# Optimization experiments

Measured on AMD Instinct MI355X. Metric: run time of the kernel, lower is better.

## Reference

```python
import jax, jax.numpy as jnp
import numpy as np

N = 20000      # nodes
E = 320000     # edges
GD = 256       # g_dim
H = 8          # head_n
D = 32         # head_d
XD = 256       # x_dim
PS = 4         # x_ps
HID = 512      # FF hidden (hardcoded in module)
EPS = 1e-5
SCALE = GD ** -0.5  # note: module scales by g_dim**-0.5, not head_d**-0.5


def layernorm(x, w, b):
    mu = jnp.mean(x, axis=-1, keepdims=True)
    var = jnp.var(x, axis=-1, keepdims=True)
    return (x - mu) * jax.lax.rsqrt(var + EPS) * w + b


def setup_inputs() -> dict:
    key = jax.random.key(0)
    ks = jax.random.split(key, 16)
    inp = {
        "x": jax.random.normal(ks[0], (N, XD, PS, PS), jnp.float32),
        "h": jax.random.normal(ks[1], (N, GD), jnp.float32),
        "src": jax.random.randint(ks[2], (E,), 0, N, jnp.int32),
        "dst": jax.random.randint(ks[3], (E,), 0, N, jnp.int32),
        # xproj conv (kernel covers full patch -> equivalent to a linear)
        "conv_w": jax.random.normal(ks[4], (GD, XD, PS, PS), jnp.float32) * 0.02,
        "conv_b": jnp.zeros((GD,), jnp.float32),
        # GraphT outer LayerNorm
        "norm_w": jnp.ones((GD,), jnp.float32),
        "norm_b": jnp.zeros((GD,), jnp.float32),
        # attention norm_in + projections
        "nin_w": jnp.ones((GD,), jnp.float32),
        "nin_b": jnp.zeros((GD,), jnp.float32),
        "w_qkv": jax.random.normal(ks[5], (3 * H * D, GD), jnp.float32) * 0.02,
        "w_out": jax.random.normal(ks[6], (GD, H * D), jnp.float32) * 0.02,
        "b_out": jnp.zeros((GD,), jnp.float32),
        # FeedForward: LayerNorm + Linear(GD,HID) + GELU + Linear(HID,GD)
        "ffn_w": jnp.ones((GD,), jnp.float32),
        "ffn_b": jnp.zeros((GD,), jnp.float32),
        "w1": jax.random.normal(ks[7], (HID, GD), jnp.float32) * 0.02,
        "b1": jnp.zeros((HID,), jnp.float32),
        "w2": jax.random.normal(ks[8], (GD, HID), jnp.float32) * 0.02,
        "b2": jnp.zeros((GD,), jnp.float32),
    }
    return inp


def reference(x, h, src, dst, conv_w, conv_b, norm_w, norm_b, nin_w, nin_b,
              w_qkv, w_out, b_out, ffn_w, ffn_b, w1, b1, w2, b2):
    # xproj: Conv2d with kernel == full spatial extent -> linear over flattened patch
    xp = x.reshape(N, XD * PS * PS) @ conv_w.reshape(GD, XD * PS * PS).T + conv_b  # [N, GD]

    hn = layernorm(h, norm_w, norm_b)  # GraphT.norm

    # --- GraphAttention ---
    s = layernorm(hn, nin_w, nin_b)                    # norm_in
    qkv = s @ w_qkv.T                                  # [N, 3*H*D]
    q, k, v = jnp.split(qkv, 3, axis=-1)
    q = q.reshape(N, H, D)
    k = k.reshape(N, H, D)
    v = v.reshape(N, H, D)

    # per-edge elementwise attention (DGL u_mul_v), scaled
    att = q[src] * k[dst] * SCALE                      # [E, H, D]
    # edge softmax over incoming edges of each destination, per (h, d) slot
    amax = jax.ops.segment_max(att, dst, num_segments=N)   # [N, H, D]
    e = jnp.exp(att - amax[dst])
    z = jax.ops.segment_sum(e, dst, num_segments=N)
    a = e / z[dst]                                     # [E, H, D]
    # weighted aggregation: sum over edges of v_src * att
    rst = jax.ops.segment_sum(v[src] * a, dst, num_segments=N)  # [N, H, D]

    attn_out = rst.reshape(N, H * D) @ w_out.T + b_out  # to_out (dropout=eval noop)

    # --- FeedForward (norm -> linear -> gelu -> linear) ---
    f = layernorm(attn_out, ffn_w, ffn_b)
    f = jax.nn.gelu(f @ w1.T + b1, approximate=False)
    f = f @ w2.T + b2

    out = f + hn + xp
    return out
```

## Files before the change

kernel.cpp:

```cpp
#include <hip/hip_runtime.h>
#include <hip/hip_bf16.h>
#include <math.h>

typedef __hip_bfloat16 bf16;
typedef __attribute__((ext_vector_type(8))) short bf16x8;
typedef __attribute__((ext_vector_type(4))) float f32x4;

#define N_NODES 20000
#define N_EDGES 320000
#define GD 256
#define HID 512
#define QKV3 768
#define SCALE 0.0625f
#define EPS 1e-5f

__device__ __forceinline__ float b2f(bf16 x) { return __bfloat162float(x); }
__device__ __forceinline__ bf16 f2b(float x) { return __float2bfloat16(x); }
__device__ __forceinline__ short f2bs(float x) {
    bf16 b = __float2bfloat16(x);
    union { bf16 b; short s; } u; u.b = b; return u.s;
}
__device__ __forceinline__ float ldf(const void* p, size_t i, int isbf) {
    return isbf ? __bfloat162float(((const bf16*)p)[i]) : ((const float*)p)[i];
}

__global__ void detect_kernel(const void* __restrict__ normw, int* __restrict__ flag) {
    if (threadIdx.x == 0) {
        unsigned short u = ((const unsigned short*)normw)[0];
        *flag = (u == 0x3F80) ? 1 : 0;
    }
}

struct ConvArgs {
    const void* src[5];
    bf16* dst[5];
    int n[5];
};
__global__ void conv_bf16_all(ConvArgs a, const int* __restrict__ flag) {
    int i = blockIdx.x * 256 + threadIdx.x;
    int fl = *flag;
    #pragma unroll
    for (int s = 0; s < 5; ++s) {
        if (i < a.n[s]) {
            a.dst[s][i] = f2b(ldf(a.src[s], i, fl));
            return;
        }
        i -= a.n[s];
    }
}

__global__ void count_kernel(const int* __restrict__ dst, int* __restrict__ deg) {
    int e = blockIdx.x * 256 + threadIdx.x;
    if (e < N_EDGES) atomicAdd(&deg[dst[e]], 1);
}

__global__ void scan_kernel(const int* __restrict__ deg, int* __restrict__ offsets,
                            int* __restrict__ cursor) {
    const int T = 1024;
    int t = threadIdx.x;
    int chunk = (N_NODES + T - 1) / T;
    int beg = t * chunk;
    int end = beg + chunk; if (end > N_NODES) end = N_NODES;
    int s = 0;
    for (int i = beg; i < end; ++i) s += deg[i];
    __shared__ int ls[T];
    ls[t] = s;
    __syncthreads();
    for (int off = 1; off < T; off <<= 1) {
        int v = (t >= off) ? ls[t - off] : 0;
        __syncthreads();
        ls[t] += v;
        __syncthreads();
    }
    int run = (t == 0) ? 0 : ls[t - 1];
    for (int i = beg; i < end; ++i) {
        offsets[i] = run; cursor[i] = run; run += deg[i];
    }
    if (t == T - 1) offsets[N_NODES] = run;
}

__global__ void fill_kernel(const int* __restrict__ src, const int* __restrict__ dst,
                            int* __restrict__ cursor, int* __restrict__ ssrc) {
    int e = blockIdx.x * 256 + threadIdx.x;
    if (e < N_EDGES) {
        int p = atomicAdd(&cursor[dst[e]], 1);
        ssrc[p] = src[e];
    }
}

__global__ void ln_fused_kernel(const void* __restrict__ h,
                                const void* __restrict__ nw, const void* __restrict__ nb,
                                const void* __restrict__ iw, const void* __restrict__ ib,
                                float* __restrict__ hn, bf16* __restrict__ s,
                                const int* __restrict__ flag) {
    int wave = threadIdx.x >> 6, lane = threadIdx.x & 63;
    int n = blockIdx.x * 4 + wave;
    int fl = *flag;
    size_t base = (size_t)n * GD;
    float x[4]; float sum = 0.f, sq = 0.f;
    #pragma unroll
    for (int i = 0; i < 4; ++i) {
        x[i] = ldf(h, base + lane + 64 * i, fl);
        sum += x[i]; sq += x[i] * x[i];
    }
    #pragma unroll
    for (int off = 32; off; off >>= 1) { sum += __shfl_xor(sum, off); sq += __shfl_xor(sq, off); }
    float mu = sum * (1.0f / GD);
    float rs = rsqrtf(sq * (1.0f / GD) - mu * mu + EPS);
    float y[4]; float s2 = 0.f, q2 = 0.f;
    #pragma unroll
    for (int i = 0; i < 4; ++i) {
        int j = lane + 64 * i;
        y[i] = (x[i] - mu) * rs * ldf(nw, j, fl) + ldf(nb, j, fl);
        hn[base + j] = y[i];
        s2 += y[i]; q2 += y[i] * y[i];
    }
    #pragma unroll
    for (int off = 32; off; off >>= 1) { s2 += __shfl_xor(s2, off); q2 += __shfl_xor(q2, off); }
    float mu2 = s2 * (1.0f / GD);
    float rs2 = rsqrtf(q2 * (1.0f / GD) - mu2 * mu2 + EPS);
    #pragma unroll
    for (int i = 0; i < 4; ++i) {
        int j = lane + 64 * i;
        s[base + j] = f2b((y[i] - mu2) * rs2 * ldf(iw, j, fl) + ldf(ib, j, fl));
    }
}

__global__ void ln_kernel(const bf16* __restrict__ in,
                          const void* __restrict__ w, const void* __restrict__ b,
                          bf16* __restrict__ out, const int* __restrict__ flag) {
    int wave = threadIdx.x >> 6, lane = threadIdx.x & 63;
    int n = blockIdx.x * 4 + wave;
    int fl = *flag;
    size_t base = (size_t)n * GD;
    float x[4]; float sum = 0.f, sq = 0.f;
    #pragma unroll
    for (int i = 0; i < 4; ++i) {
        x[i] = b2f(in[base + lane + 64 * i]);
        sum += x[i]; sq += x[i] * x[i];
    }
    #pragma unroll
    for (int off = 32; off; off >>= 1) { sum += __shfl_xor(sum, off); sq += __shfl_xor(sq, off); }
    float mu = sum * (1.0f / GD);
    float rs = rsqrtf(sq * (1.0f / GD) - mu * mu + EPS);
    #pragma unroll
    for (int i = 0; i < 4; ++i) {
        int j = lane + 64 * i;
        out[base + j] = f2b((x[i] - mu) * rs * ldf(w, j, fl) + ldf(b, j, fl));
    }
}

__global__ void attn_kernel(const bf16* __restrict__ qkv, const int* __restrict__ offsets,
                            const int* __restrict__ ssrc, bf16* __restrict__ rst) {
    int n = blockIdx.x;
    int j = threadIdx.x;
    float kj = b2f(qkv[(size_t)n * QKV3 + GD + j]) * SCALE;
    int beg = offsets[n], end = offsets[n + 1];
    float m = -INFINITY, l = 0.f, acc = 0.f;
    for (int e = beg; e < end; ++e) {
        int sI = ssrc[e];
        const bf16* qrow = qkv + (size_t)sI * QKV3;
        float a = b2f(qrow[j]) * kj;
        float vv = b2f(qrow[2 * GD + j]);
        float mn = fmaxf(m, a);
        float c = __expf(m - mn);
        float p = __expf(a - mn);
        l = l * c + p;
        acc = acc * c + p * vv;
        m = mn;
    }
    rst[(size_t)n * GD + j] = f2b(end > beg ? acc / l : 0.f);
}

template<int EPI, int DYNA>
__launch_bounds__(256)
__global__ void gemm_bt(const void* __restrict__ A, const bf16* __restrict__ B,
                        const void* __restrict__ bias, void* __restrict__ Cout,
                        const float* __restrict__ add0, const float* __restrict__ add1,
                        int M, int Nn, int K, const int* __restrict__ flag) {
    constexpr int BM = 128, BN = 128, BK = 64, LDW = BK + 8;
    __shared__ bf16 As[BM * LDW];
    __shared__ bf16 Bs[BN * LDW];
    const int m0 = blockIdx.x * BM;
    const int n0 = blockIdx.y * BN;
    const int tid = threadIdx.x;
    const int lane = tid & 63;
    const int wave = tid >> 6;
    const int quad = lane >> 4;
    const int l16 = lane & 15;
    const int wm = (wave & 1) * 64;
    const int wn = (wave >> 1) * 64;
    const int fl = *flag;

    const int kc = K / gridDim.z;
    const int kbeg = blockIdx.z * kc;
    const int kend = kbeg + kc;

    f32x4 acc[4][4] = {};

    for (int k0 = kbeg; k0 < kend; k0 += BK) {
        #pragma unroll
        for (int p = 0; p < 4; ++p) {
            int l = p * 256 + tid;
            int row = l >> 3;
            int ko = (l & 7) * 8;
            int gr = m0 + row; gr = gr < M ? gr : M - 1;
            if (!DYNA || fl) {
                *(int4*)(&As[row * LDW + ko]) =
                    *(const int4*)((const bf16*)A + (size_t)gr * K + k0 + ko);
            } else {
                const float* Af = (const float*)A + (size_t)gr * K + k0 + ko;
                float4 lo = *(const float4*)(Af);
                float4 hi = *(const float4*)(Af + 4);
                bf16x8 v;
                v[0] = f2bs(lo.x); v[1] = f2bs(lo.y); v[2] = f2bs(lo.z); v[3] = f2bs(lo.w);
                v[4] = f2bs(hi.x); v[5] = f2bs(hi.y); v[6] = f2bs(hi.z); v[7] = f2bs(hi.w);
                *(bf16x8*)(&As[row * LDW + ko]) = v;
            }
            *(int4*)(&Bs[row * LDW + ko]) = *(const int4*)(B + (size_t)(n0 + row) * K + k0 + ko);
        }
        __syncthreads();
        #pragma unroll
        for (int kk = 0; kk < BK; kk += 32) {
            bf16x8 af[4], bfm[4];
            #pragma unroll
            for (int i = 0; i < 4; ++i)
                af[i] = *(const bf16x8*)(&As[(wm + i * 16 + l16) * LDW + kk + quad * 8]);
            #pragma unroll
            for (int j = 0; j < 4; ++j)
                bfm[j] = *(const bf16x8*)(&Bs[(wn + j * 16 + l16) * LDW + kk + quad * 8]);
            #pragma unroll
            for (int i = 0; i < 4; ++i)
                #pragma unroll
                for (int j = 0; j < 4; ++j)
                    acc[i][j] = __builtin_amdgcn_mfma_f32_16x16x32_bf16(af[i], bfm[j], acc[i][j], 0, 0, 0);
        }
        __syncthreads();
    }

    #pragma unroll
    for (int i = 0; i < 4; ++i) {
        #pragma unroll
        for (int j = 0; j < 4; ++j) {
            int col = n0 + wn + j * 16 + l16;
            float bv = bias ? ldf(bias, col, fl) : 0.0f;
            if (EPI == 4 && blockIdx.z != 0) bv = 0.0f;
            #pragma unroll
            for (int r = 0; r < 4; ++r) {
                int gr = m0 + wm + i * 16 + quad * 4 + r;
                if (gr >= M) continue;
                float v = acc[i][j][r] + bv;
                size_t idx = (size_t)gr * Nn + col;
                if (EPI == 2) v = 0.5f * v * (1.0f + erff(v * 0.70710678118f));
                if (EPI == 3) v += add0[idx] + add1[idx];
                if (EPI == 0)      ((float*)Cout)[idx] = v;
                else if (EPI == 3) { if (fl) ((bf16*)Cout)[idx] = f2b(v); else ((float*)Cout)[idx] = v; }
                else if (EPI == 4) atomicAdd(&((float*)Cout)[idx], v);
                else               ((bf16*)Cout)[idx] = f2b(v);
            }
        }
    }
}

extern "C" void kernel_launch(void* const* d_in, const int* in_sizes, int n_in,
                              void* d_out, int out_size, void* d_ws, size_t ws_size,
                              hipStream_t stream) {
    const void* x      = d_in[0];
    const void* h      = d_in[1];
    const int*  src    = (const int*)d_in[2];
    const int*  dst    = (const int*)d_in[3];
    const void* conv_w = d_in[4];
    const void* conv_b = d_in[5];
    const void* norm_w = d_in[6];
    const void* norm_b = d_in[7];
    const void* nin_w  = d_in[8];
    const void* nin_b  = d_in[9];
    const void* w_qkv  = d_in[10];
    const void* w_out  = d_in[11];
    const void* b_out  = d_in[12];
    const void* ffn_w  = d_in[13];
    const void* ffn_b  = d_in[14];
    const void* w1     = d_in[15];
    const void* b1     = d_in[16];
    const void* w2     = d_in[17];
    const void* b2     = d_in[18];

    char* w = (char*)d_ws;
    float* xp   = (float*)w; w += (size_t)N_NODES * GD * 4;
    float* hn   = (float*)w; w += (size_t)N_NODES * GD * 4;
    bf16*  s    = (bf16*)w;  w += (size_t)N_NODES * GD * 2;
    bf16*  qkv  = (bf16*)w;  w += (size_t)N_NODES * QKV3 * 2;
    bf16*  rst  = (bf16*)w;  w += (size_t)N_NODES * GD * 2;
    bf16*  attn = (bf16*)w;  w += (size_t)N_NODES * GD * 2;
    bf16*  cw    = (bf16*)w; w += (size_t)4096 * 256 * 2;
    bf16*  wqkvb = (bf16*)w; w += (size_t)768 * 256 * 2;
    bf16*  woutb = (bf16*)w; w += (size_t)256 * 256 * 2;
    bf16*  w1b   = (bf16*)w; w += (size_t)512 * 256 * 2;
    bf16*  w2b   = (bf16*)w; w += (size_t)256 * 512 * 2;
    int* deg     = (int*)w;  w += (size_t)N_NODES * 4;
    int* cursor  = (int*)w;  w += (size_t)N_NODES * 4;
    int* offsets = (int*)w;  w += (size_t)(N_NODES + 4) * 4;
    int* ssrc    = (int*)w;  w += (size_t)N_EDGES * 4;
    int* flag    = (int*)w;  w += 16;
    bf16* fln = s;
    bf16* f1  = qkv;

    detect_kernel<<<1, 64, 0, stream>>>(norm_w, flag);
    ConvArgs ca;
    ca.src[0] = conv_w; ca.dst[0] = cw;    ca.n[0] = 4096 * 256;
    ca.src[1] = w_qkv;  ca.dst[1] = wqkvb; ca.n[1] = 768 * 256;
    ca.src[2] = w_out;  ca.dst[2] = woutb; ca.n[2] = 256 * 256;
    ca.src[3] = w1;     ca.dst[3] = w1b;   ca.n[3] = 512 * 256;
    ca.src[4] = w2;     ca.dst[4] = w2b;   ca.n[4] = 256 * 512;
    int conv_total = ca.n[0] + ca.n[1] + ca.n[2] + ca.n[3] + ca.n[4];
    conv_bf16_all<<<(conv_total + 255) / 256, 256, 0, stream>>>(ca, flag);

    hipMemsetAsync(deg, 0, N_NODES * sizeof(int), stream);
    count_kernel<<<(N_EDGES + 255) / 256, 256, 0, stream>>>(dst, deg);
    scan_kernel<<<1, 1024, 0, stream>>>(deg, offsets, cursor);
    fill_kernel<<<(N_EDGES + 255) / 256, 256, 0, stream>>>(src, dst, cursor, ssrc);

    ln_fused_kernel<<<N_NODES / 4, 256, 0, stream>>>(h, norm_w, norm_b, nin_w, nin_b, hn, s, flag);

    dim3 blk(256);
    hipMemsetAsync(xp, 0, (size_t)N_NODES * GD * 4, stream);
    gemm_bt<4, 1><<<dim3(157, 2, 4), blk, 0, stream>>>(x, cw, conv_b, xp, nullptr, nullptr, N_NODES, GD, 4096, flag);
    gemm_bt<1, 0><<<dim3(157, 6), blk, 0, stream>>>(s, wqkvb, nullptr, qkv, nullptr, nullptr, N_NODES, QKV3, GD, flag);
    attn_kernel<<<N_NODES, 256, 0, stream>>>(qkv, offsets, ssrc, rst);
    gemm_bt<1, 0><<<dim3(157, 2), blk, 0, stream>>>(rst, woutb, b_out, attn, nullptr, nullptr, N_NODES, GD, GD, flag);
    ln_kernel<<<N_NODES / 4, 256, 0, stream>>>(attn, ffn_w, ffn_b, fln, flag);
    gemm_bt<2, 0><<<dim3(157, 4), blk, 0, stream>>>(fln, w1b, b1, f1, nullptr, nullptr, N_NODES, HID, GD, flag);
    gemm_bt<3, 0><<<dim3(157, 2), blk, 0, stream>>>(f1, w2b, b2, d_out, xp, hn, N_NODES, GD, HID, flag);
}
```

Before: 950.2 us.

## Add dedicated fp32-input xproj GEMM with async LDS loads and double buffering

Adds a specialised kernel for the x-projection GEMM when inputs are fp32. It streams fp32 A tiles directly into LDS with global_load_lds using an XOR swizzle, double-buffers A and B, and converts to bf16 at fragment load time before MFMA. The generic gemm_bt path now exits early in fp32 mode and runs only for bf16 inputs. The aim is to overlap the dominant 4096-deep load stream with compute, at the cost of doubling LDS footprint and an extra kernel launch that does nothing.

```diff
diff --git a/kernel.cpp b/kernel.cpp
--- a/kernel.cpp
+++ b/kernel.cpp
@@ -11,6 +11,7 @@
 #define GD 256
 #define HID 512
 #define QKV3 768
+#define XK 4096
 #define SCALE 0.0625f
 #define EPS 1e-5f
 
@@ -22,6 +23,12 @@
 }
 __device__ __forceinline__ float ldf(const void* p, size_t i, int isbf) {
     return isbf ? __bfloat162float(((const bf16*)p)[i]) : ((const float*)p)[i];
+}
+
+typedef __attribute__((address_space(3))) void lds_void;
+typedef __attribute__((address_space(1))) void glb_void;
+__device__ __forceinline__ void gload_lds16(const void* g, void* l) {
+    __builtin_amdgcn_global_load_lds((const glb_void*)g, (lds_void*)l, 16, 0, 0);
 }
 
 __global__ void detect_kernel(const void* __restrict__ normw, int* __restrict__ flag) {
@@ -172,12 +179,117 @@
     rst[(size_t)n * GD + j] = f2b(end > beg ? acc / l : 0.f);
 }
 
+__launch_bounds__(256, 3)
+__global__ void xproj_kernel(const float* __restrict__ A, const bf16* __restrict__ B,
+                             const float* __restrict__ bias, float* __restrict__ C,
+                             const int* __restrict__ flag) {
+    if (*flag) return;
+    constexpr int BM = 128, BK = 32;
+    __shared__ __align__(16) float As[2][BM * BK];
+    __shared__ __align__(16) bf16  Bs[2][BM][BK + 8];
+    const int m0 = blockIdx.x * BM;
+    const int n0 = blockIdx.y * BM;
+    const int tid = threadIdx.x;
+    const int lane = tid & 63;
+    const int wave = tid >> 6;
+    const int quad = lane >> 4;
+    const int l16 = lane & 15;
+    const int wm = (wave & 1) * 64;
+    const int wn = (wave >> 1) * 64;
+    const int kc = XK / gridDim.z;
+    const int kbeg = blockIdx.z * kc;
+    const int nt = kc / BK;
+
+    f32x4 acc[4][4] = {};
+    int4 breg[2];
+
+    auto stageA = [&](int buf, int k0) {
+        #pragma unroll
+        for (int s = 0; s < 4; ++s) {
+            int row = wave * 32 + s * 8 + (lane >> 3);
+            int gslot = (lane & 7) ^ (row & 7);
+            int gr = m0 + row; if (gr >= N_NODES) gr = N_NODES - 1;
+            gload_lds16(A + (size_t)gr * XK + k0 + gslot * 4,
+                        &As[buf][(wave * 4 + s) * 256]);
+        }
+    };
+    auto loadB = [&](int k0) {
+        #pragma unroll
+        for (int u = 0; u < 2; ++u) {
+            int c = tid * 2 + u;
+            int row = c >> 2, slot = c & 3;
+            breg[u] = *(const int4*)((const char*)B + ((size_t)(n0 + row) * XK + k0) * 2 + slot * 16);
+        }
+    };
+    auto writeB = [&](int buf) {
+        #pragma unroll
+        for (int u = 0; u < 2; ++u) {
+            int c = tid * 2 + u;
+            int row = c >> 2, slot = c & 3;
+            *(int4*)(&Bs[buf][row][slot * 8]) = breg[u];
+        }
+    };
+
+    loadB(kbeg);
+    stageA(0, kbeg);
+    writeB(0);
+    __syncthreads();
+
+    int buf = 0;
+    for (int t = 0; t < nt; ++t) {
+        if (t + 1 < nt) {
+            loadB(kbeg + (t + 1) * BK);
+            stageA(buf ^ 1, kbeg + (t + 1) * BK);
+        }
+        const f32x4* ap = (const f32x4*)As[buf];
+        bf16x8 af[4], bfm[4];
+        #pragma unroll
+        for (int i = 0; i < 4; ++i) {
+            int r = wm + i * 16 + l16;
+            f32x4 a0 = ap[r * 8 + ((quad * 2) ^ (r & 7))];
+            f32x4 a1 = ap[r * 8 + ((quad * 2 + 1) ^ (r & 7))];
+            bf16x8 v;
+            v[0] = f2bs(a0[0]); v[1] = f2bs(a0[1]); v[2] = f2bs(a0[2]); v[3] = f2bs(a0[3]);
+            v[4] = f2bs(a1[0]); v[5] = f2bs(a1[1]); v[6] = f2bs(a1[2]); v[7] = f2bs(a1[3]);
+            af[i] = v;
+        }
+        #pragma unroll
+        for (int j = 0; j < 4; ++j)
+            bfm[j] = *(const bf16x8*)(&Bs[buf][wn + j * 16 + l16][quad * 8]);
+        #pragma unroll
+        for (int i = 0; i < 4; ++i)
+            #pragma unroll
+            for (int j = 0; j < 4; ++j)
+                acc[i][j] = __builtin_amdgcn_mfma_f32_16x16x32_bf16(af[i], bfm[j], acc[i][j], 0, 0, 0);
+        if (t + 1 < nt) writeB(buf ^ 1);
+        __syncthreads();
+        buf ^= 1;
+    }
+
+    #pragma unroll
+    for (int i = 0; i < 4; ++i) {
+        #pragma unroll
+        for (int j = 0; j < 4; ++j) {
+            int col = n0 + wn + j * 16 + l16;
+            float bv = (blockIdx.z == 0) ? bias[col] : 0.0f;
+            #pragma unroll
+            for (int r = 0; r < 4; ++r) {
+                int gr = m0 + wm + i * 16 + quad * 4 + r;
+                if (gr >= N_NODES) continue;
+                atomicAdd(&C[(size_t)gr * GD + col], acc[i][j][r] + bv);
+            }
+        }
+    }
+}
+
 template<int EPI, int DYNA>
 __launch_bounds__(256)
 __global__ void gemm_bt(const void* __restrict__ A, const bf16* __restrict__ B,
                         const void* __restrict__ bias, void* __restrict__ Cout,
                         const float* __restrict__ add0, const float* __restrict__ add1,
                         int M, int Nn, int K, const int* __restrict__ flag) {
+    const int fl = *flag;
+    if (DYNA == 2 && fl == 0) return;
     constexpr int BM = 128, BN = 128, BK = 64, LDW = BK + 8;
     __shared__ bf16 As[BM * LDW];
     __shared__ bf16 Bs[BN * LDW];
@@ -190,7 +302,6 @@
     const int l16 = lane & 15;
     const int wm = (wave & 1) * 64;
     const int wn = (wave >> 1) * 64;
-    const int fl = *flag;
 
     const int kc = K / gridDim.z;
     const int kbeg = blockIdx.z * kc;
@@ -324,7 +435,8 @@
 
     dim3 blk(256);
     hipMemsetAsync(xp, 0, (size_t)N_NODES * GD * 4, stream);
-    gemm_bt<4, 1><<<dim3(157, 2, 4), blk, 0, stream>>>(x, cw, conv_b, xp, nullptr, nullptr, N_NODES, GD, 4096, flag);
+    xproj_kernel<<<dim3(157, 2, 4), blk, 0, stream>>>((const float*)x, cw, (const float*)conv_b, xp, flag);
+    gemm_bt<4, 2><<<dim3(157, 2, 4), blk, 0, stream>>>(x, cw, conv_b, xp, nullptr, nullptr, N_NODES, GD, 4096, flag);
     gemm_bt<1, 0><<<dim3(157, 6), blk, 0, stream>>>(s, wqkvb, nullptr, qkv, nullptr, nullptr, N_NODES, QKV3, GD, flag);
     attn_kernel<<<N_NODES, 256, 0, stream>>>(qkv, offsets, ssrc, rst);
     gemm_bt<1, 0><<<dim3(157, 2), blk, 0, stream>>>(rst, woutb, b_out, attn, nullptr, nullptr, N_NODES, GD, GD, flag);
```

Result: slower. 1.000 ms (+5.3%).

## Add register-only MFMA xproj kernel with pre-tiled conv weights for fp32 inputs

Applied to the files above, without the earlier changes.

Adds a register-only MFMA kernel for the xproj GEMM, used when inputs are fp32. It reads the fp32 x rows directly, converts them to bf16 in registers, and reads B from a weight copy pre-arranged into MFMA fragment order, so no LDS is used. Each wave covers 32 rows by all 256 columns, so x is read once instead of once per N tile as in the two-column-block grid. The bf16-input path keeps the old gemm_bt, which now exits early in the fp32 case. The cost is an extra weight copy, more atomics per element on split-K, and high register pressure from 32 accumulator vectors.

```diff
diff --git a/kernel.cpp b/kernel.cpp
--- a/kernel.cpp
+++ b/kernel.cpp
@@ -11,6 +11,7 @@
 #define GD 256
 #define HID 512
 #define QKV3 768
+#define XK 4096
 #define SCALE 0.0625f
 #define EPS 1e-5f
 
@@ -36,13 +37,20 @@
     bf16* dst[5];
     int n[5];
 };
-__global__ void conv_bf16_all(ConvArgs a, const int* __restrict__ flag) {
+__global__ void conv_bf16_all(ConvArgs a, const int* __restrict__ flag, bf16* __restrict__ cwt) {
     int i = blockIdx.x * 256 + threadIdx.x;
     int fl = *flag;
     #pragma unroll
     for (int s = 0; s < 5; ++s) {
         if (i < a.n[s]) {
-            a.dst[s][i] = f2b(ldf(a.src[s], i, fl));
+            float v = ldf(a.src[s], i, fl);
+            a.dst[s][i] = f2b(v);
+            if (s == 0) {
+                int r = i >> 12;
+                int k = i & 4095;
+                int T = k >> 5, slot = (k >> 3) & 3, e = k & 7;
+                cwt[((size_t)T << 13) + (slot << 11) + (r << 3) + e] = f2b(v);
+            }
             return;
         }
         i -= a.n[s];
@@ -172,12 +180,76 @@
     rst[(size_t)n * GD + j] = f2b(end > beg ? acc / l : 0.f);
 }
 
+__launch_bounds__(256, 2)
+__global__ void xproj_reg(const float* __restrict__ A, const bf16* __restrict__ Bt,
+                          const float* __restrict__ bias, float* __restrict__ C,
+                          const int* __restrict__ flag) {
+    if (*flag) return;
+    const int lane = threadIdx.x & 63;
+    const int wave = threadIdx.x >> 6;
+    const int q = lane >> 4;
+    const int l16 = lane & 15;
+    const int wrow = blockIdx.x * 128 + wave * 32;
+    const int kc = XK / gridDim.z;
+    const int kbeg = blockIdx.z * kc;
+    const int nt = kc / 32;
+
+    f32x4 acc[2][16] = {};
+
+    int r0 = wrow + l16;      if (r0 >= N_NODES) r0 = N_NODES - 1;
+    int r1 = wrow + 16 + l16; if (r1 >= N_NODES) r1 = N_NODES - 1;
+    const float* pa0 = A + (size_t)r0 * XK + kbeg + q * 8;
+    const float* pa1 = A + (size_t)r1 * XK + kbeg + q * 8;
+    const bf16* pb = Bt + ((size_t)(kbeg >> 5) << 13) + (q << 11) + (l16 << 3);
+
+    float4 a0lo = *(const float4*)(pa0), a0hi = *(const float4*)(pa0 + 4);
+    float4 a1lo = *(const float4*)(pa1), a1hi = *(const float4*)(pa1 + 4);
+
+    #pragma unroll 2
+    for (int t = 0; t < nt; ++t) {
+        bf16x8 af0, af1;
+        af0[0] = f2bs(a0lo.x); af0[1] = f2bs(a0lo.y); af0[2] = f2bs(a0lo.z); af0[3] = f2bs(a0lo.w);
+        af0[4] = f2bs(a0hi.x); af0[5] = f2bs(a0hi.y); af0[6] = f2bs(a0hi.z); af0[7] = f2bs(a0hi.w);
+        af1[0] = f2bs(a1lo.x); af1[1] = f2bs(a1lo.y); af1[2] = f2bs(a1lo.z); af1[3] = f2bs(a1lo.w);
+        af1[4] = f2bs(a1hi.x); af1[5] = f2bs(a1hi.y); af1[6] = f2bs(a1hi.z); af1[7] = f2bs(a1hi.w);
+        if (t + 1 < nt) {
+            pa0 += 32; pa1 += 32;
+            a0lo = *(const float4*)(pa0); a0hi = *(const float4*)(pa0 + 4);
+            a1lo = *(const float4*)(pa1); a1hi = *(const float4*)(pa1 + 4);
+        }
+        #pragma unroll
+        for (int j = 0; j < 16; ++j) {
+            bf16x8 bfm = *(const bf16x8*)(pb + j * 128);
+            acc[0][j] = __builtin_amdgcn_mfma_f32_16x16x32_bf16(af0, bfm, acc[0][j], 0, 0, 0);
+            acc[1][j] = __builtin_amdgcn_mfma_f32_16x16x32_bf16(af1, bfm, acc[1][j], 0, 0, 0);
+        }
+        pb += 8192;
+    }
+
+    #pragma unroll
+    for (int i = 0; i < 2; ++i) {
+        #pragma unroll
+        for (int j = 0; j < 16; ++j) {
+            int col = j * 16 + l16;
+            float bv = (blockIdx.z == 0) ? bias[col] : 0.0f;
+            #pragma unroll
+            for (int r = 0; r < 4; ++r) {
+                int gr = wrow + i * 16 + q * 4 + r;
+                if (gr >= N_NODES) continue;
+                atomicAdd(&C[(size_t)gr * GD + col], acc[i][j][r] + bv);
+            }
+        }
+    }
+}
+
 template<int EPI, int DYNA>
 __launch_bounds__(256)
 __global__ void gemm_bt(const void* __restrict__ A, const bf16* __restrict__ B,
                         const void* __restrict__ bias, void* __restrict__ Cout,
                         const float* __restrict__ add0, const float* __restrict__ add1,
                         int M, int Nn, int K, const int* __restrict__ flag) {
+    const int fl = *flag;
+    if (DYNA == 2 && fl == 0) return;
     constexpr int BM = 128, BN = 128, BK = 64, LDW = BK + 8;
     __shared__ bf16 As[BM * LDW];
     __shared__ bf16 Bs[BN * LDW];
@@ -190,7 +262,6 @@
     const int l16 = lane & 15;
     const int wm = (wave & 1) * 64;
     const int wn = (wave >> 1) * 64;
-    const int fl = *flag;
 
     const int kc = K / gridDim.z;
     const int kbeg = blockIdx.z * kc;
@@ -293,6 +364,7 @@
     bf16*  rst  = (bf16*)w;  w += (size_t)N_NODES * GD * 2;
     bf16*  attn = (bf16*)w;  w += (size_t)N_NODES * GD * 2;
     bf16*  cw    = (bf16*)w; w += (size_t)4096 * 256 * 2;
+    bf16*  cwt   = (bf16*)w; w += (size_t)4096 * 256 * 2;
     bf16*  wqkvb = (bf16*)w; w += (size_t)768 * 256 * 2;
     bf16*  woutb = (bf16*)w; w += (size_t)256 * 256 * 2;
     bf16*  w1b   = (bf16*)w; w += (size_t)512 * 256 * 2;
@@ -313,7 +385,7 @@
     ca.src[3] = w1;     ca.dst[3] = w1b;   ca.n[3] = 512 * 256;
     ca.src[4] = w2;     ca.dst[4] = w2b;   ca.n[4] = 256 * 512;
     int conv_total = ca.n[0] + ca.n[1] + ca.n[2] + ca.n[3] + ca.n[4];
-    conv_bf16_all<<<(conv_total + 255) / 256, 256, 0, stream>>>(ca, flag);
+    conv_bf16_all<<<(conv_total + 255) / 256, 256, 0, stream>>>(ca, flag, cwt);
 
     hipMemsetAsync(deg, 0, N_NODES * sizeof(int), stream);
     count_kernel<<<(N_EDGES + 255) / 256, 256, 0, stream>>>(dst, deg);
@@ -324,7 +396,8 @@
 
     dim3 blk(256);
     hipMemsetAsync(xp, 0, (size_t)N_NODES * GD * 4, stream);
-    gemm_bt<4, 1><<<dim3(157, 2, 4), blk, 0, stream>>>(x, cw, conv_b, xp, nullptr, nullptr, N_NODES, GD, 4096, flag);
+    xproj_reg<<<dim3(157, 1, 4), blk, 0, stream>>>((const float*)x, cwt, (const float*)conv_b, xp, flag);
+    gemm_bt<4, 2><<<dim3(157, 2, 4), blk, 0, stream>>>(x, cw, conv_b, xp, nullptr, nullptr, N_NODES, GD, 4096, flag);
     gemm_bt<1, 0><<<dim3(157, 6), blk, 0, stream>>>(s, wqkvb, nullptr, qkv, nullptr, nullptr, N_NODES, QKV3, GD, flag);
     attn_kernel<<<N_NODES, 256, 0, stream>>>(qkv, offsets, ssrc, rst);
     gemm_bt<1, 0><<<dim3(157, 2), blk, 0, stream>>>(rst, woutb, b_out, attn, nullptr, nullptr, N_NODES, GD, GD, flag);
```

Result: slower. 1.118 ms (+17.6%).
